# Optimization experiments

Measured on AMD Instinct MI355X. Metric: run time of the kernel, lower is better.

Reference implementation:

```python
import jax, jax.numpy as jnp
import numpy as np

EMBED_DIM = 512

def _equalized_linear(x, W):
    # StyleGAN equalized LR: effective weight = W / sqrt(fan_in); out = x @ W_eff.T
    c = 1.0 / np.sqrt(W.shape[1])
    return jnp.einsum('bnd,ed->bne', x, W) * c

def setup_inputs() -> dict:
    key = jax.random.key(0)
    ks = jax.random.split(key, 6)
    B, N, D = 16, 2048, 512
    return {
        'q': jax.random.normal(ks[0], (B, N, D), dtype=jnp.float32),
        'k': jax.random.normal(ks[1], (B, N, D), dtype=jnp.float32),
        'v': jax.random.normal(ks[2], (B, N, D), dtype=jnp.float32),
        'Wq': jax.random.normal(ks[3], (EMBED_DIM, D), dtype=jnp.float32),
        'Wk': jax.random.normal(ks[4], (EMBED_DIM, D), dtype=jnp.float32),
        'Wv': jax.random.normal(ks[5], (EMBED_DIM, D), dtype=jnp.float32),
    }

def reference(q, k, v, Wq, Wk, Wv):
    scale = EMBED_DIM ** (-0.5)
    qp = _equalized_linear(q, Wq)  # [B,Nq,E]
    kp = _equalized_linear(k, Wk)  # [B,Nk,E]
    vp = _equalized_linear(v, Wv)  # [B,Nk,E]
    dots = jnp.einsum('bqe,bke->bqk', qp, kp) * scale  # [B,Nq,Nk]
    attn = jax.nn.softmax(dots, axis=-1)
    out = jnp.einsum('bqk,bke->bqe', attn, vp)  # [B,Nq,E]
    return (out, attn)
```

## Files before the change

### kernel.cpp

```cpp
#include <hip/hip_runtime.h>
#include <hip/hip_bf16.h>

typedef __attribute__((ext_vector_type(8))) short short8;
typedef __attribute__((ext_vector_type(4))) float floatx4;

#define LDP 72
#define TP  136
#define PP  40

#define ATTN_OFF ((size_t)16 * 2048 * 512)

__device__ __forceinline__ unsigned short f2bf(float f) {
    union { __hip_bfloat16 h; unsigned short u; } cv;
    cv.h = __float2bfloat16(f);
    return cv.u;
}

__device__ __forceinline__ uint2 f4_to_bf4(float x, float y, float z, float w) {
    uint2 r;
    r.x = (unsigned)f2bf(x) | ((unsigned)f2bf(y) << 16);
    r.y = (unsigned)f2bf(z) | ((unsigned)f2bf(w) << 16);
    return r;
}

__global__ __launch_bounds__(256, 2)
void proj_kernel(const float* __restrict__ q, const float* __restrict__ k,
                 const float* __restrict__ v, const float* __restrict__ wq,
                 const float* __restrict__ wk, const float* __restrict__ wv,
                 unsigned short* __restrict__ qp, unsigned short* __restrict__ kp,
                 unsigned short* __restrict__ vpT)
{
    const int mat = blockIdx.z;
    const float* __restrict__ x = (mat == 0) ? q : (mat == 1) ? k : v;
    const float* __restrict__ w = (mat == 0) ? wq : (mat == 1) ? wk : wv;
    const float scale = (mat == 0) ? (1.0f / 512.0f) : 0.044194173824159216f;

    const int m0 = blockIdx.x * 128;
    const int n0 = blockIdx.y * 128;

    __shared__ __align__(16) unsigned short sm[2 * 128 * LDP];
    unsigned short* lds_a = sm;
    unsigned short* lds_b = sm + 128 * LDP;
    unsigned short* lds_t = sm;

    const int t = threadIdx.x;
    const int wave = t >> 6, ln = t & 15, qd = (t >> 4) & 3;
    const int wm = wave >> 1, wn = wave & 1;

    floatx4 acc[4][4];
    for (int mi = 0; mi < 4; ++mi)
        for (int ni = 0; ni < 4; ++ni)
            acc[mi][ni] = (floatx4){0.f, 0.f, 0.f, 0.f};

    for (int kb = 0; kb < 512; kb += 64) {
        for (int i = 0; i < 8; ++i) {
            int lin = t + 256 * i;
            int row = lin >> 4, c4 = lin & 15;
            const float4 a4 = *(const float4*)&x[(size_t)(m0 + row) * 512 + kb + c4 * 4];
            *(uint2*)&lds_a[row * LDP + c4 * 4] = f4_to_bf4(a4.x, a4.y, a4.z, a4.w);
            const float4 b4 = *(const float4*)&w[(size_t)(n0 + row) * 512 + kb + c4 * 4];
            *(uint2*)&lds_b[row * LDP + c4 * 4] = f4_to_bf4(b4.x, b4.y, b4.z, b4.w);
        }
        __syncthreads();
        for (int kk = 0; kk < 2; ++kk) {
            short8 af[4], bg[4];
            for (int mi = 0; mi < 4; ++mi)
                af[mi] = *(const short8*)&lds_a[(wm * 64 + mi * 16 + ln) * LDP + kk * 32 + qd * 8];
            for (int ni = 0; ni < 4; ++ni)
                bg[ni] = *(const short8*)&lds_b[(wn * 64 + ni * 16 + ln) * LDP + kk * 32 + qd * 8];
            for (int mi = 0; mi < 4; ++mi)
                for (int ni = 0; ni < 4; ++ni)
                    acc[mi][ni] = __builtin_amdgcn_mfma_f32_16x16x32_bf16(
                        af[mi], bg[ni], acc[mi][ni], 0, 0, 0);
        }
        __syncthreads();
    }

    for (int mi = 0; mi < 4; ++mi)
        for (int ni = 0; ni < 4; ++ni)
            for (int r = 0; r < 4; ++r) {
                float val = acc[mi][ni][r] * scale;
                int row = wm * 64 + mi * 16 + qd * 4 + r;
                int col = wn * 64 + ni * 16 + ln;
                if (mat == 2) lds_t[col * TP + row] = f2bf(val);
                else          lds_t[row * TP + col] = f2bf(val);
            }
    __syncthreads();
    if (mat < 2) {
        unsigned short* dst = (mat == 0) ? qp : kp;
        for (int i = 0; i < 8; ++i) {
            int lin = t + 256 * i;
            int row = lin >> 4, c8 = lin & 15;
            *(uint4*)&dst[(size_t)(m0 + row) * 512 + n0 + c8 * 8] =
                *(const uint4*)&lds_t[row * TP + c8 * 8];
        }
    } else {
        int b = m0 >> 11;
        int tloc = m0 & 2047;
        for (int i = 0; i < 8; ++i) {
            int lin = t + 256 * i;
            int row = lin >> 4, c8 = lin & 15;
            *(uint4*)&vpT[(size_t)b * 512 * 2048 + (size_t)(n0 + row) * 2048 + tloc + c8 * 8] =
                *(const uint4*)&lds_t[row * TP + c8 * 8];
        }
    }
}

__global__ __launch_bounds__(256, 2)
void dots_kernel(const unsigned short* __restrict__ qp, const unsigned short* __restrict__ kp,
                 float* __restrict__ attn, float* __restrict__ lsum)
{
    const int b = blockIdx.z;
    const int row0 = blockIdx.y * 128;
    const int col0 = blockIdx.x * 128;

    __shared__ __align__(16) unsigned short sm[2 * 128 * LDP];
    unsigned short* lds_a = sm;
    unsigned short* lds_b = sm + 128 * LDP;
    __shared__ float lds_l[128];

    const int t = threadIdx.x;
    const int wave = t >> 6, ln = t & 15, qd = (t >> 4) & 3;
    const int wm = wave >> 1, wn = wave & 1;

    if (t < 128) lds_l[t] = 0.f;

    const unsigned short* arow = qp + (size_t)(b * 2048 + row0) * 512;
    const unsigned short* brow = kp + (size_t)(b * 2048 + col0) * 512;

    floatx4 acc[4][4];
    for (int mi = 0; mi < 4; ++mi)
        for (int ni = 0; ni < 4; ++ni)
            acc[mi][ni] = (floatx4){0.f, 0.f, 0.f, 0.f};

    for (int kb = 0; kb < 512; kb += 64) {
        for (int i = 0; i < 4; ++i) {
            int lin = t + 256 * i;
            int row = lin >> 3, c8 = lin & 7;
            *(uint4*)&lds_a[row * LDP + c8 * 8] = *(const uint4*)&arow[(size_t)row * 512 + kb + c8 * 8];
            *(uint4*)&lds_b[row * LDP + c8 * 8] = *(const uint4*)&brow[(size_t)row * 512 + kb + c8 * 8];
        }
        __syncthreads();
        for (int kk = 0; kk < 2; ++kk) {
            short8 af[4], bg[4];
            for (int mi = 0; mi < 4; ++mi)
                af[mi] = *(const short8*)&lds_a[(wm * 64 + mi * 16 + ln) * LDP + kk * 32 + qd * 8];
            for (int ni = 0; ni < 4; ++ni)
                bg[ni] = *(const short8*)&lds_b[(wn * 64 + ni * 16 + ln) * LDP + kk * 32 + qd * 8];
            for (int mi = 0; mi < 4; ++mi)
                for (int ni = 0; ni < 4; ++ni)
                    acc[mi][ni] = __builtin_amdgcn_mfma_f32_16x16x32_bf16(
                        af[mi], bg[ni], acc[mi][ni], 0, 0, 0);
        }
        __syncthreads();
    }

    float* attnb = attn + (size_t)(b * 2048 + row0) * 2048 + col0;
    for (int mi = 0; mi < 4; ++mi) {
        float s[4] = {0.f, 0.f, 0.f, 0.f};
        for (int ni = 0; ni < 4; ++ni) {
            int colL = wn * 64 + ni * 16 + ln;
            for (int r = 0; r < 4; ++r) {
                float p = __expf(acc[mi][ni][r]);
                int rowL = wm * 64 + mi * 16 + qd * 4 + r;
                attnb[(size_t)rowL * 2048 + colL] = p;
                s[r] += p;
            }
        }
        for (int r = 0; r < 4; ++r) {
            float vv = s[r];
            vv += __shfl_xor(vv, 1);
            vv += __shfl_xor(vv, 2);
            vv += __shfl_xor(vv, 4);
            vv += __shfl_xor(vv, 8);
            if (ln == 0) atomicAdd(&lds_l[wm * 64 + mi * 16 + qd * 4 + r], vv);
        }
    }
    __syncthreads();
    if (t < 128) atomicAdd(&lsum[b * 2048 + row0 + t], lds_l[t]);
}

__global__ __launch_bounds__(512, 2)
void out_kernel(const unsigned short* __restrict__ vpT, float* __restrict__ attn,
                const float* __restrict__ lsum, float* __restrict__ out)
{
    const int b  = blockIdx.x;
    const int r0 = blockIdx.y * 128;

    __shared__ __align__(16) unsigned short p_lds[2][128 * PP];

    const int t = threadIdx.x;
    const int wave = t >> 6, ln = t & 15, qd = (t >> 4) & 3;
    const int wm = wave >> 2, wn = wave & 3;

    const int prow = t >> 2;
    const int pcol = (t & 3) * 8;
    const float il = 1.0f / lsum[b * 2048 + r0 + prow];

    float* pbase = attn + (size_t)(b * 2048 + r0 + prow) * 2048 + pcol;
    const unsigned short* vb = vpT + (size_t)b * 512 * 2048;

    floatx4 acc[4][8];
    #pragma unroll
    for (int mi = 0; mi < 4; ++mi)
        #pragma unroll
        for (int ni = 0; ni < 8; ++ni)
            acc[mi][ni] = (floatx4){0.f, 0.f, 0.f, 0.f};

    {
        float4 pa = *(const float4*)(pbase);
        float4 pb = *(const float4*)(pbase + 4);
        pa.x *= il; pa.y *= il; pa.z *= il; pa.w *= il;
        pb.x *= il; pb.y *= il; pb.z *= il; pb.w *= il;
        *(float4*)(pbase)     = pa;
        *(float4*)(pbase + 4) = pb;
        uint2 lo = f4_to_bf4(pa.x, pa.y, pa.z, pa.w);
        uint2 hi = f4_to_bf4(pb.x, pb.y, pb.z, pb.w);
        uint4 pk = {lo.x, lo.y, hi.x, hi.y};
        *(uint4*)&p_lds[0][prow * PP + pcol] = pk;
    }

    for (int i = 0; i < 64; ++i) {
        const int kc = i * 32;
        const int buf = i & 1;
        __syncthreads();

        short8 bg[8];
        #pragma unroll
        for (int ni = 0; ni < 8; ++ni)
            bg[ni] = *(const short8*)&vb[(size_t)(wn * 128 + ni * 16 + ln) * 2048 + kc + qd * 8];

        float4 pa, pb;
        if (i < 63) {
            pa = *(const float4*)(pbase + kc + 32);
            pb = *(const float4*)(pbase + kc + 36);
        }

        short8 af[4];
        #pragma unroll
        for (int mi = 0; mi < 4; ++mi)
            af[mi] = *(const short8*)&p_lds[buf][(wm * 64 + mi * 16 + ln) * PP + qd * 8];

        #pragma unroll
        for (int ni = 0; ni < 8; ++ni)
            #pragma unroll
            for (int mi = 0; mi < 4; ++mi)
                acc[mi][ni] = __builtin_amdgcn_mfma_f32_16x16x32_bf16(
                    af[mi], bg[ni], acc[mi][ni], 0, 0, 0);

        if (i < 63) {
            pa.x *= il; pa.y *= il; pa.z *= il; pa.w *= il;
            pb.x *= il; pb.y *= il; pb.z *= il; pb.w *= il;
            *(float4*)(pbase + kc + 32) = pa;
            *(float4*)(pbase + kc + 36) = pb;
            uint2 lo = f4_to_bf4(pa.x, pa.y, pa.z, pa.w);
            uint2 hi = f4_to_bf4(pb.x, pb.y, pb.z, pb.w);
            uint4 pk = {lo.x, lo.y, hi.x, hi.y};
            *(uint4*)&p_lds[buf ^ 1][prow * PP + pcol] = pk;
        }
    }

    float* outb = out + (size_t)(b * 2048 + r0) * 512;
    #pragma unroll
    for (int mi = 0; mi < 4; ++mi)
        #pragma unroll
        for (int ni = 0; ni < 8; ++ni) {
            int col = wn * 128 + ni * 16 + ln;
            #pragma unroll
            for (int r = 0; r < 4; ++r) {
                int row = wm * 64 + mi * 16 + qd * 4 + r;
                outb[(size_t)row * 512 + col] = acc[mi][ni][r];
            }
        }
}

extern "C" void kernel_launch(void* const* d_in, const int* in_sizes, int n_in,
                              void* d_out, int out_size, void* d_ws, size_t ws_size,
                              hipStream_t stream) {
    const float* q  = (const float*)d_in[0];
    const float* k  = (const float*)d_in[1];
    const float* v  = (const float*)d_in[2];
    const float* wq = (const float*)d_in[3];
    const float* wk = (const float*)d_in[4];
    const float* wv = (const float*)d_in[5];

    unsigned short* qp  = (unsigned short*)d_ws;
    unsigned short* kp  = qp + (size_t)32768 * 512;
    unsigned short* vpT = kp + (size_t)32768 * 512;
    float* lsum = (float*)(vpT + (size_t)16 * 512 * 2048);

    float* out  = (float*)d_out;
    float* attn = out + ATTN_OFF;

    hipMemsetAsync(lsum, 0, (size_t)16 * 2048 * sizeof(float), stream);

    proj_kernel<<<dim3(256, 4, 3), 256, 0, stream>>>(q, k, v, wq, wk, wv, qp, kp, vpT);
    dots_kernel<<<dim3(16, 16, 16), 256, 0, stream>>>(qp, kp, attn, lsum);
    out_kernel<<<dim3(16, 16), 512, 0, stream>>>(vpT, attn, lsum, out);
}
```

Measured before the change: 916.4 us.

## Halve out_kernel row tile to 64 to double block count and occupancy

Reduce the out_kernel tile from 128 to 64 query rows per block and drop the row-wave split, so each of the 8 waves covers 64 output columns for all 64 rows. This doubles the grid, cuts accumulator registers per thread, and allows 4 blocks per CU to improve latency hiding on the streaming attn normalize/rewrite. The cost is halved reuse of the V tiles, which doubles V reads from L2/HBM, and narrower per-thread attn accesses.

```diff
diff --git a/kernel.cpp b/kernel.cpp
--- a/kernel.cpp
+++ b/kernel.cpp
@@ -180,44 +180,39 @@
     if (t < 128) atomicAdd(&lsum[b * 2048 + row0 + t], lds_l[t]);
 }
 
-__global__ __launch_bounds__(512, 2)
+__global__ __launch_bounds__(512, 4)
 void out_kernel(const unsigned short* __restrict__ vpT, float* __restrict__ attn,
                 const float* __restrict__ lsum, float* __restrict__ out)
 {
     const int b  = blockIdx.x;
-    const int r0 = blockIdx.y * 128;
-
-    __shared__ __align__(16) unsigned short p_lds[2][128 * PP];
+    const int r0 = blockIdx.y * 64;
+
+    __shared__ __align__(16) unsigned short p_lds[2][64 * PP];
 
     const int t = threadIdx.x;
     const int wave = t >> 6, ln = t & 15, qd = (t >> 4) & 3;
-    const int wm = wave >> 2, wn = wave & 3;
-
-    const int prow = t >> 2;
-    const int pcol = (t & 3) * 8;
+    const int wn = wave;
+
+    const int prow = t >> 3;
+    const int pcol = (t & 7) * 4;
     const float il = 1.0f / lsum[b * 2048 + r0 + prow];
 
     float* pbase = attn + (size_t)(b * 2048 + r0 + prow) * 2048 + pcol;
     const unsigned short* vb = vpT + (size_t)b * 512 * 2048;
 
-    floatx4 acc[4][8];
+    floatx4 acc[4][4];
     #pragma unroll
     for (int mi = 0; mi < 4; ++mi)
         #pragma unroll
-        for (int ni = 0; ni < 8; ++ni)
+        for (int ni = 0; ni < 4; ++ni)
             acc[mi][ni] = (floatx4){0.f, 0.f, 0.f, 0.f};
 
     {
         float4 pa = *(const float4*)(pbase);
-        float4 pb = *(const float4*)(pbase + 4);
         pa.x *= il; pa.y *= il; pa.z *= il; pa.w *= il;
-        pb.x *= il; pb.y *= il; pb.z *= il; pb.w *= il;
-        *(float4*)(pbase)     = pa;
-        *(float4*)(pbase + 4) = pb;
-        uint2 lo = f4_to_bf4(pa.x, pa.y, pa.z, pa.w);
-        uint2 hi = f4_to_bf4(pb.x, pb.y, pb.z, pb.w);
-        uint4 pk = {lo.x, lo.y, hi.x, hi.y};
-        *(uint4*)&p_lds[0][prow * PP + pcol] = pk;
+        *(float4*)(pbase) = pa;
+        uint2 pk = f4_to_bf4(pa.x, pa.y, pa.z, pa.w);
+        *(uint2*)&p_lds[0][prow * PP + pcol] = pk;
     }
 
     for (int i = 0; i < 64; ++i) {
@@ -225,24 +220,21 @@
         const int buf = i & 1;
         __syncthreads();
 
-        short8 bg[8];
-        #pragma unroll
-        for (int ni = 0; ni < 8; ++ni)
-            bg[ni] = *(const short8*)&vb[(size_t)(wn * 128 + ni * 16 + ln) * 2048 + kc + qd * 8];
-
-        float4 pa, pb;
-        if (i < 63) {
-            pa = *(const float4*)(pbase + kc + 32);
-            pb = *(const float4*)(pbase + kc + 36);
-        }
+        float4 pa;
+        if (i < 63) pa = *(const float4*)(pbase + kc + 32);
+
+        short8 bg[4];
+        #pragma unroll
+        for (int ni = 0; ni < 4; ++ni)
+            bg[ni] = *(const short8*)&vb[(size_t)(wn * 64 + ni * 16 + ln) * 2048 + kc + qd * 8];
 
         short8 af[4];
         #pragma unroll
         for (int mi = 0; mi < 4; ++mi)
-            af[mi] = *(const short8*)&p_lds[buf][(wm * 64 + mi * 16 + ln) * PP + qd * 8];
-
-        #pragma unroll
-        for (int ni = 0; ni < 8; ++ni)
+            af[mi] = *(const short8*)&p_lds[buf][(mi * 16 + ln) * PP + qd * 8];
+
+        #pragma unroll
+        for (int ni = 0; ni < 4; ++ni)
             #pragma unroll
             for (int mi = 0; mi < 4; ++mi)
                 acc[mi][ni] = __builtin_amdgcn_mfma_f32_16x16x32_bf16(
@@ -250,13 +242,9 @@
 
         if (i < 63) {
             pa.x *= il; pa.y *= il; pa.z *= il; pa.w *= il;
-            pb.x *= il; pb.y *= il; pb.z *= il; pb.w *= il;
             *(float4*)(pbase + kc + 32) = pa;
-            *(float4*)(pbase + kc + 36) = pb;
-            uint2 lo = f4_to_bf4(pa.x, pa.y, pa.z, pa.w);
-            uint2 hi = f4_to_bf4(pb.x, pb.y, pb.z, pb.w);
-            uint4 pk = {lo.x, lo.y, hi.x, hi.y};
-            *(uint4*)&p_lds[buf ^ 1][prow * PP + pcol] = pk;
+            uint2 pk = f4_to_bf4(pa.x, pa.y, pa.z, pa.w);
+            *(uint2*)&p_lds[buf ^ 1][prow * PP + pcol] = pk;
         }
     }
 
@@ -264,11 +252,11 @@
     #pragma unroll
     for (int mi = 0; mi < 4; ++mi)
         #pragma unroll
-        for (int ni = 0; ni < 8; ++ni) {
-            int col = wn * 128 + ni * 16 + ln;
+        for (int ni = 0; ni < 4; ++ni) {
+            int col = wn * 64 + ni * 16 + ln;
             #pragma unroll
             for (int r = 0; r < 4; ++r) {
-                int row = wm * 64 + mi * 16 + qd * 4 + r;
+                int row = mi * 16 + qd * 4 + r;
                 outb[(size_t)row * 512 + col] = acc[mi][ni][r];
             }
         }
@@ -296,5 +284,5 @@
 
     proj_kernel<<<dim3(256, 4, 3), 256, 0, stream>>>(q, k, v, wq, wk, wv, qp, kp, vpT);
     dots_kernel<<<dim3(16, 16, 16), 256, 0, stream>>>(qp, kp, attn, lsum);
-    out_kernel<<<dim3(16, 16), 512, 0, stream>>>(vpT, attn, lsum, out);
-}
+    out_kernel<<<dim3(16, 32), 512, 0, stream>>>(vpT, attn, lsum, out);
+}
```

Result: no change. 902.5 us (-1.5%).
